# Kernel tuning notes

Hardware: AMD Instinct MI355X
Metric: run time of the kernel (lower is better)

The kernel has to match this reference:

```python
import jax, jax.numpy as jnp
import numpy as np

EPS = 1e-5

def _layer_norm(x, gamma, beta):
    mu = jnp.mean(x, axis=-1, keepdims=True)
    var = jnp.mean(jnp.square(x - mu), axis=-1, keepdims=True)
    return (x - mu) * jax.lax.rsqrt(var + EPS) * gamma + beta

def setup_inputs() -> dict:
    key = jax.random.key(0)
    ks = jax.random.split(key, 6)
    B, D, H = 8192, 1024, 1024
    x = jax.random.normal(ks[0], (B, D), dtype=jnp.float32)
    h0 = jax.random.normal(ks[1], (B, H), dtype=jnp.float32)
    c0 = jax.random.normal(ks[2], (B, H), dtype=jnp.float32)
    # learned params (orthogonal init approximated by scaled normal for reference purposes)
    weight_h = jax.random.normal(ks[3], (H, 4 * H), dtype=jnp.float32) / np.sqrt(H)
    weight_x = jax.random.normal(ks[4], (D, 4 * H), dtype=jnp.float32) / np.sqrt(D)
    bias = jnp.zeros((4 * H,), dtype=jnp.float32).at[:H].set(1.0)  # forget-gate bias init to 1
    ln1_g = jnp.ones((4 * H,), jnp.float32); ln1_b = jnp.zeros((4 * H,), jnp.float32)
    ln2_g = jnp.ones((4 * H,), jnp.float32); ln2_b = jnp.zeros((4 * H,), jnp.float32)
    ln3_g = jnp.ones((H,), jnp.float32); ln3_b = jnp.zeros((H,), jnp.float32)
    return {"x": x, "h0": h0, "c0": c0, "weight_h": weight_h, "weight_x": weight_x,
            "bias": bias, "ln1_g": ln1_g, "ln1_b": ln1_b, "ln2_g": ln2_g, "ln2_b": ln2_b,
            "ln3_g": ln3_g, "ln3_b": ln3_b}

def reference(x, h0, c0, weight_h, weight_x, bias, ln1_g, ln1_b, ln2_g, ln2_b, ln3_g, ln3_b):
    # gates: [B, 4H] = LN(h0 @ Wh) + LN(x @ Wx) + bias
    gates = _layer_norm(h0 @ weight_h, ln1_g, ln1_b) + _layer_norm(x @ weight_x, ln2_g, ln2_b) + bias
    H = h0.shape[-1]
    f_g, i_g, o_g, c_g = jnp.split(gates, 4, axis=1)  # forget, in, out, cell
    c1 = jax.nn.sigmoid(f_g) * c0 + jax.nn.sigmoid(i_g) * jnp.tanh(c_g)
    h1 = jax.nn.sigmoid(o_g) * jnp.tanh(_layer_norm(c1, ln3_g, ln3_b))
    return (h1, c1)
```

## Files before the change

### kernel.cpp

```cpp
#include <hip/hip_runtime.h>
#include <cstdint>

#define B_ROWS 8192
#define KDIM 1024
#define N4 4096

typedef __attribute__((ext_vector_type(8))) short short8;
typedef __attribute__((ext_vector_type(4))) float float4v;

__device__ __forceinline__ unsigned short f2bf(float f) {
  union { float f; unsigned int u; } v; v.f = f;
  unsigned int r = v.u + 0x7fffu + ((v.u >> 16) & 1u);
  return (unsigned short)(r >> 16);
}

__device__ __forceinline__ float bf2f(unsigned short s) {
  union { unsigned int u; float f; } v; v.u = ((unsigned int)s) << 16;
  return v.f;
}

__device__ __forceinline__ void async16(const unsigned short* g, unsigned short* l) {
  auto gp = (const __attribute__((address_space(1))) unsigned int*)(uintptr_t)g;
  auto lp = (__attribute__((address_space(3))) unsigned int*)(unsigned int)(uintptr_t)l;
  __builtin_amdgcn_global_load_lds(gp, lp, 16, 0, 0);
}

__device__ __forceinline__ float sigm(float v) {
  return __builtin_amdgcn_rcpf(1.f + __builtin_amdgcn_exp2f(-1.44269504088896f * v));
}
__device__ __forceinline__ float tanh_f(float v) {
  return 1.f - 2.f * __builtin_amdgcn_rcpf(1.f + __builtin_amdgcn_exp2f(2.88539008177793f * v));
}


__global__ __launch_bounds__(256) void cast_bf16(const float* __restrict__ in0,
                                                 unsigned short* __restrict__ out0,
                                                 const float* __restrict__ in1,
                                                 unsigned short* __restrict__ out1) {
  const float* in = blockIdx.y ? in1 : in0;
  unsigned short* out = blockIdx.y ? out1 : out0;
  int i = (blockIdx.x * 256 + threadIdx.x) * 4;
  float4 v = *(const float4*)(in + i);
  ushort4 o;
  o.x = f2bf(v.x); o.y = f2bf(v.y); o.z = f2bf(v.z); o.w = f2bf(v.w);
  *(ushort4*)(out + i) = o;
}

__global__ __launch_bounds__(256) void transpose_cast(const float* __restrict__ W0,
                                                      unsigned short* __restrict__ Wt0,
                                                      const float* __restrict__ W1,
                                                      unsigned short* __restrict__ Wt1) {
  const float* W = blockIdx.z ? W1 : W0;
  unsigned short* Wt = blockIdx.z ? Wt1 : Wt0;
  __shared__ float tile[32][33];
  int n0 = blockIdx.x * 32;
  int k0 = blockIdx.y * 32;
  int tx = threadIdx.x & 31;
  int ty = threadIdx.x >> 5;
#pragma unroll
  for (int i = 0; i < 32; i += 8)
    tile[ty + i][tx] = W[(size_t)(k0 + ty + i) * N4 + n0 + tx];
  __syncthreads();
#pragma unroll
  for (int i = 0; i < 32; i += 8)
    Wt[(size_t)(n0 + ty + i) * KDIM + k0 + tx] = f2bf(tile[tx][ty + i]);
}


#define BAR()    asm volatile("s_barrier" ::: "memory")
#define LGKM0()  asm volatile("s_waitcnt lgkmcnt(0)" ::: "memory")
#define VM4BAR() asm volatile("s_waitcnt vmcnt(4)\n\ts_barrier" ::: "memory")
#define SCHED0() __builtin_amdgcn_sched_barrier(0)

__global__ __launch_bounds__(512, 2) void gemm_bf16(
    const unsigned short* __restrict__ Ah, const unsigned short* __restrict__ Wth,
    unsigned short* __restrict__ Uh,
    const unsigned short* __restrict__ Ax, const unsigned short* __restrict__ Wtx,
    unsigned short* __restrict__ Ux, int row0) {
  const unsigned short* A; const unsigned short* W; unsigned short* U;
  if (blockIdx.z == 0) { A = Ah; W = Wth; U = Uh; } else { A = Ax; W = Wtx; U = Ux; }

  __shared__ unsigned short ldsA[2 * 256 * 64];
  __shared__ unsigned short ldsB[2 * 256 * 64];

  const int tid = threadIdx.x;
  const int wave = tid >> 6;
  const int lane = tid & 63;
  const int wm2 = wave >> 2;
  const int wn4 = wave & 3;

  const int gx = N4 / 256;
  const int nwg = gx * (int)gridDim.y;
  const int f = (int)blockIdx.y * gx + (int)blockIdx.x;
  const int qq = nwg >> 3, rr = nwg & 7;
  const int xcd = f & 7, idx = f >> 3;
  const int wg = (xcd < rr) ? (xcd * (qq + 1) + idx)
                            : (rr * (qq + 1) + (xcd - rr) * qq + idx);
  const int bx = wg & (gx - 1);
  const int by = wg / gx;

  const int m0 = row0 + by * 256;
  const int n0 = bx * 256;

  const int r8 = lane >> 3;
  const int c8 = lane & 7;
  const int g8 = ((c8 - r8) & 7) * 8;
  const int aE = (wave & 3) * 16 + (wave >> 2) * 128;
  const int aL = aE + 64;
  const int bE = (wave >> 1) * 64 + (wave & 1) * 16;
  const int bL = bE + 32;

  const unsigned short* gAe = A + (size_t)(m0 + aE + r8) * KDIM + g8;
  const unsigned short* gAl = A + (size_t)(m0 + aL + r8) * KDIM + g8;
  const unsigned short* gBe = W + (size_t)(n0 + bE + r8) * KDIM + g8;
  const unsigned short* gBl = W + (size_t)(n0 + bL + r8) * KDIM + g8;

  const int lq = lane & 15, lh = lane >> 4;
  const int offA0 = (wm2 * 128 + lq) * 64 + ((lh + lq) & 7) * 8;
  const int offA1 = (wm2 * 128 + lq) * 64 + ((4 + lh + lq) & 7) * 8;
  const int offB0 = (wn4 * 64 + lq) * 64 + ((lh + lq) & 7) * 8;
  const int offB1 = (wn4 * 64 + lq) * 64 + ((4 + lh + lq) & 7) * 8;

  float4v acc[8][4];
  float4v zero = {0.f, 0.f, 0.f, 0.f};
#pragma unroll
  for (int i = 0; i < 8; ++i)
#pragma unroll
    for (int j = 0; j < 4; ++j) acc[i][j] = zero;

#define STAGE2(gptr, lbase, kk)                                   \
  do {                                                            \
    async16((gptr) + (kk), (lbase));                              \
    async16((gptr) + (kk) + 8 * KDIM, (lbase) + 8 * 64);          \
  } while (0)

  STAGE2(gAe, ldsA + aE * 64, 0);
  STAGE2(gBe, ldsB + bE * 64, 0);
  STAGE2(gBl, ldsB + bL * 64, 0);
  STAGE2(gAl, ldsA + aL * 64, 0);
  VM4BAR();

  short8 aF[4][2], bF[4][2];

#pragma unroll 2
  for (int t = 0; t < KDIM / 64; ++t) {
    const unsigned short* sA = ldsA + (t & 1) * 16384;
    const unsigned short* sB = ldsB + (t & 1) * 16384;
    unsigned short* nA = (unsigned short*)ldsA + ((t + 1) & 1) * 16384;
    unsigned short* nB = (unsigned short*)ldsB + ((t + 1) & 1) * 16384;
    const int kNX = (t + 1) * 64;

#pragma unroll
    for (int mi = 0; mi < 4; ++mi) {
      aF[mi][0] = *(const short8*)(sA + offA0 + mi * 1024);
      aF[mi][1] = *(const short8*)(sA + offA1 + mi * 1024);
    }
#pragma unroll
    for (int ni = 0; ni < 2; ++ni) {
      bF[ni][0] = *(const short8*)(sB + offB0 + ni * 1024);
      bF[ni][1] = *(const short8*)(sB + offB1 + ni * 1024);
    }
    STAGE2(gAe, nA + aE * 64, kNX);
    BAR(); LGKM0(); SCHED0();
    __builtin_amdgcn_s_setprio(1);
#pragma unroll
    for (int kk = 0; kk < 2; ++kk)
#pragma unroll
      for (int mi = 0; mi < 4; ++mi)
#pragma unroll
        for (int ni = 0; ni < 2; ++ni)
          acc[mi][ni] = __builtin_amdgcn_mfma_f32_16x16x32_bf16(aF[mi][kk], bF[ni][kk], acc[mi][ni], 0, 0, 0);
    __builtin_amdgcn_s_setprio(0);
    SCHED0();
    VM4BAR();

#pragma unroll
    for (int ni = 0; ni < 2; ++ni) {
      bF[2 + ni][0] = *(const short8*)(sB + offB0 + (2 + ni) * 1024);
      bF[2 + ni][1] = *(const short8*)(sB + offB1 + (2 + ni) * 1024);
    }
    STAGE2(gBe, nB + bE * 64, kNX);
    BAR(); LGKM0(); SCHED0();
    __builtin_amdgcn_s_setprio(1);
#pragma unroll
    for (int kk = 0; kk < 2; ++kk)
#pragma unroll
      for (int mi = 0; mi < 4; ++mi)
#pragma unroll
        for (int ni = 0; ni < 2; ++ni)
          acc[mi][2 + ni] = __builtin_amdgcn_mfma_f32_16x16x32_bf16(aF[mi][kk], bF[2 + ni][kk], acc[mi][2 + ni], 0, 0, 0);
    __builtin_amdgcn_s_setprio(0);
    SCHED0();
    VM4BAR();

#pragma unroll
    for (int mi = 0; mi < 4; ++mi) {
      aF[mi][0] = *(const short8*)(sA + offA0 + (4 + mi) * 1024);
      aF[mi][1] = *(const short8*)(sA + offA1 + (4 + mi) * 1024);
    }
    STAGE2(gBl, nB + bL * 64, kNX);
    BAR(); LGKM0(); SCHED0();
    __builtin_amdgcn_s_setprio(1);
#pragma unroll
    for (int kk = 0; kk < 2; ++kk)
#pragma unroll
      for (int mi = 0; mi < 4; ++mi)
#pragma unroll
        for (int ni = 0; ni < 2; ++ni)
          acc[4 + mi][ni] = __builtin_amdgcn_mfma_f32_16x16x32_bf16(aF[mi][kk], bF[ni][kk], acc[4 + mi][ni], 0, 0, 0);
    __builtin_amdgcn_s_setprio(0);
    SCHED0();
    BAR();

    STAGE2(gAl, nA + aL * 64, kNX);
    BAR(); SCHED0();
    __builtin_amdgcn_s_setprio(1);
#pragma unroll
    for (int kk = 0; kk < 2; ++kk)
#pragma unroll
      for (int mi = 0; mi < 4; ++mi)
#pragma unroll
        for (int ni = 0; ni < 2; ++ni)
          acc[4 + mi][2 + ni] = __builtin_amdgcn_mfma_f32_16x16x32_bf16(aF[mi][kk], bF[2 + ni][kk], acc[4 + mi][2 + ni], 0, 0, 0);
    __builtin_amdgcn_s_setprio(0);
    SCHED0();
    VM4BAR();
  }
  asm volatile("s_waitcnt vmcnt(0)" ::: "memory");

  const int colc = lane & 15;
  const int rowq = (lane >> 4) * 4;
  unsigned short* Ub = U + (size_t)(by * 256 + wm2 * 128 + rowq) * N4 + n0 + wn4 * 64 + colc;
#pragma unroll
  for (int mi = 0; mi < 8; ++mi)
#pragma unroll
    for (int r = 0; r < 4; ++r) {
      unsigned short* Urow = Ub + (size_t)(mi * 16 + r) * N4;
#pragma unroll
      for (int ni = 0; ni < 4; ++ni) Urow[ni * 16] = f2bf(acc[mi][ni][r]);
    }
}


__global__ __launch_bounds__(256) void fused_ln_lstm(
    const unsigned short* __restrict__ Uh, const unsigned short* __restrict__ Ux,
    const float* __restrict__ c0, const float* __restrict__ bias,
    const float* __restrict__ g1, const float* __restrict__ b1,
    const float* __restrict__ g2, const float* __restrict__ b2,
    const float* __restrict__ g3, const float* __restrict__ b3,
    float* __restrict__ h1o, float* __restrict__ c1o, int row0) {
  const int t = threadIdx.x;
  const int lane = t & 63;
  const int wv = t >> 6;
  const size_t rloc = blockIdx.x;
  const size_t rabs = rloc + (size_t)row0;

  const ushort4* uh = (const ushort4*)(Uh + rloc * N4);
  const ushort4* ux = (const ushort4*)(Ux + rloc * N4);
  float4 cold = ((const float4*)(c0 + rabs * KDIM))[t];

  float4 vh[4], vx[4];
  float sh = 0.f, qh = 0.f, sx = 0.f, qx = 0.f;
#pragma unroll
  for (int k = 0; k < 4; ++k) {
    ushort4 au = uh[k * 256 + t];
    float4 a; a.x = bf2f(au.x); a.y = bf2f(au.y); a.z = bf2f(au.z); a.w = bf2f(au.w);
    vh[k] = a;
    sh += (a.x + a.y) + (a.z + a.w);
    qh += a.x * a.x + a.y * a.y + a.z * a.z + a.w * a.w;
    ushort4 bu = ux[k * 256 + t];
    float4 b; b.x = bf2f(bu.x); b.y = bf2f(bu.y); b.z = bf2f(bu.z); b.w = bf2f(bu.w);
    vx[k] = b;
    sx += (b.x + b.y) + (b.z + b.w);
    qx += b.x * b.x + b.y * b.y + b.z * b.z + b.w * b.w;
  }
  __shared__ float red[4][4];
#pragma unroll
  for (int o = 32; o > 0; o >>= 1) {
    sh += __shfl_down(sh, o); qh += __shfl_down(qh, o);
    sx += __shfl_down(sx, o); qx += __shfl_down(qx, o);
  }
  if (lane == 0) { red[wv][0] = sh; red[wv][1] = qh; red[wv][2] = sx; red[wv][3] = qx; }
  __syncthreads();
  sh = red[0][0] + red[1][0] + red[2][0] + red[3][0];
  qh = red[0][1] + red[1][1] + red[2][1] + red[3][1];
  sx = red[0][2] + red[1][2] + red[2][2] + red[3][2];
  qx = red[0][3] + red[1][3] + red[2][3] + red[3][3];
  const float inv4 = 1.f / 4096.f;
  const float muh = sh * inv4, mux = sx * inv4;
  const float rsh = rsqrtf(qh * inv4 - muh * muh + 1e-5f);
  const float rsx = rsqrtf(qx * inv4 - mux * mux + 1e-5f);

  float4 gate[4];
#pragma unroll
  for (int k = 0; k < 4; ++k) {
    int j = k * 256 + t;
    float4 G1 = ((const float4*)g1)[j], B1 = ((const float4*)b1)[j];
    float4 G2 = ((const float4*)g2)[j], B2 = ((const float4*)b2)[j];
    float4 BB = ((const float4*)bias)[j];
    float4 a = vh[k], b = vx[k], r;
    r.x = (a.x - muh) * rsh * G1.x + B1.x + (b.x - mux) * rsx * G2.x + B2.x + BB.x;
    r.y = (a.y - muh) * rsh * G1.y + B1.y + (b.y - mux) * rsx * G2.y + B2.y + BB.y;
    r.z = (a.z - muh) * rsh * G1.z + B1.z + (b.z - mux) * rsx * G2.z + B2.z + BB.z;
    r.w = (a.w - muh) * rsh * G1.w + B1.w + (b.w - mux) * rsx * G2.w + B2.w + BB.w;
    gate[k] = r;
  }
  float4 fg = gate[0], ig = gate[1], og = gate[2], cg = gate[3];
  float4 c1v;
  c1v.x = sigm(fg.x) * cold.x + sigm(ig.x) * tanh_f(cg.x);
  c1v.y = sigm(fg.y) * cold.y + sigm(ig.y) * tanh_f(cg.y);
  c1v.z = sigm(fg.z) * cold.z + sigm(ig.z) * tanh_f(cg.z);
  c1v.w = sigm(fg.w) * cold.w + sigm(ig.w) * tanh_f(cg.w);

  float sc = (c1v.x + c1v.y) + (c1v.z + c1v.w);
  float qc = c1v.x * c1v.x + c1v.y * c1v.y + c1v.z * c1v.z + c1v.w * c1v.w;
#pragma unroll
  for (int o = 32; o > 0; o >>= 1) { sc += __shfl_down(sc, o); qc += __shfl_down(qc, o); }
  __syncthreads();
  if (lane == 0) { red[wv][0] = sc; red[wv][1] = qc; }
  __syncthreads();
  sc = red[0][0] + red[1][0] + red[2][0] + red[3][0];
  qc = red[0][1] + red[1][1] + red[2][1] + red[3][1];
  const float invH = 1.f / 1024.f;
  const float muc = sc * invH;
  const float rsc = rsqrtf(qc * invH - muc * muc + 1e-5f);
  float4 G3 = ((const float4*)g3)[t], B3 = ((const float4*)b3)[t];
  float4 h1v;
  h1v.x = sigm(og.x) * tanh_f((c1v.x - muc) * rsc * G3.x + B3.x);
  h1v.y = sigm(og.y) * tanh_f((c1v.y - muc) * rsc * G3.y + B3.y);
  h1v.z = sigm(og.z) * tanh_f((c1v.z - muc) * rsc * G3.z + B3.z);
  h1v.w = sigm(og.w) * tanh_f((c1v.w - muc) * rsc * G3.w + B3.w);

  ((float4*)(h1o + rabs * KDIM))[t] = h1v;
  ((float4*)(c1o + rabs * KDIM))[t] = c1v;
}


extern "C" void kernel_launch(void* const* d_in, const int* in_sizes, int n_in,
                              void* d_out, int out_size, void* d_ws, size_t ws_size,
                              hipStream_t stream) {
  const float* x    = (const float*)d_in[0];
  const float* h0   = (const float*)d_in[1];
  const float* c0   = (const float*)d_in[2];
  const float* Wh   = (const float*)d_in[3];
  const float* Wx   = (const float*)d_in[4];
  const float* bias = (const float*)d_in[5];
  const float* g1   = (const float*)d_in[6];
  const float* b1   = (const float*)d_in[7];
  const float* g2   = (const float*)d_in[8];
  const float* b2   = (const float*)d_in[9];
  const float* g3   = (const float*)d_in[10];
  const float* b3   = (const float*)d_in[11];
  float* h1o = (float*)d_out;
  float* c1o = h1o + (size_t)B_ROWS * KDIM;

  unsigned short* Ah  = (unsigned short*)d_ws;
  unsigned short* Ax  = Ah + (size_t)B_ROWS * KDIM;
  unsigned short* Wth = Ax + (size_t)B_ROWS * KDIM;
  unsigned short* Wtx = Wth + (size_t)N4 * KDIM;
  unsigned short* U = Wtx + (size_t)N4 * KDIM;
  size_t used = ((size_t)B_ROWS * KDIM * 2 + (size_t)N4 * KDIM * 2) * sizeof(unsigned short);
  size_t rem = ws_size > used ? ws_size - used : 0;
  int chunk = (int)(rem / ((size_t)2 * N4 * sizeof(unsigned short)));
  chunk &= ~255;
  if (chunk > B_ROWS) chunk = B_ROWS;
  if (chunk < 256) chunk = 256;

  cast_bf16<<<dim3(B_ROWS * KDIM / 1024, 2), 256, 0, stream>>>(h0, Ah, x, Ax);
  transpose_cast<<<dim3(N4 / 32, KDIM / 32, 2), 256, 0, stream>>>(Wh, Wth, Wx, Wtx);

  for (int r0 = 0; r0 < B_ROWS; r0 += chunk) {
    int rows = chunk;
    if (r0 + rows > B_ROWS) rows = B_ROWS - r0;
    unsigned short* Uh = U;
    unsigned short* Ux = U + (size_t)rows * N4;
    gemm_bf16<<<dim3(N4 / 256, rows / 256, 2), 512, 0, stream>>>(Ah, Wth, Uh, Ax, Wtx, Ux, r0);
    fused_ln_lstm<<<rows, 256, 0, stream>>>(Uh, Ux, c0, bias, g1, b1, g2, b2, g3, b3, h1o, c1o, r0);
  }
}
```

Before: 366.7 us.

## Restructure GEMM main loop into two phases with deeper B prefetch

The GEMM inner loop goes from four sub-phases with partial fragment loads and barriers to two phases per K-tile. Each phase loads all A/B fragments for one k-half, and each wave stages 32 contiguous rows. B tiles are now prefetched two iterations ahead and A one ahead, which cuts barriers and waitcnts per iteration. Separately, the bf16 cast kernel and the weight transpose-cast kernel are merged into one launch. The cost is more fragment registers held per wave and a changed overlap pattern between loads and MFMAs.

```diff
diff --git a/kernel.cpp b/kernel.cpp
--- a/kernel.cpp
+++ b/kernel.cpp
@@ -33,44 +33,45 @@
 }
 
 
-__global__ __launch_bounds__(256) void cast_bf16(const float* __restrict__ in0,
-                                                 unsigned short* __restrict__ out0,
-                                                 const float* __restrict__ in1,
-                                                 unsigned short* __restrict__ out1) {
-  const float* in = blockIdx.y ? in1 : in0;
-  unsigned short* out = blockIdx.y ? out1 : out0;
-  int i = (blockIdx.x * 256 + threadIdx.x) * 4;
-  float4 v = *(const float4*)(in + i);
-  ushort4 o;
-  o.x = f2bf(v.x); o.y = f2bf(v.y); o.z = f2bf(v.z); o.w = f2bf(v.w);
-  *(ushort4*)(out + i) = o;
-}
-
-__global__ __launch_bounds__(256) void transpose_cast(const float* __restrict__ W0,
-                                                      unsigned short* __restrict__ Wt0,
-                                                      const float* __restrict__ W1,
-                                                      unsigned short* __restrict__ Wt1) {
-  const float* W = blockIdx.z ? W1 : W0;
-  unsigned short* Wt = blockIdx.z ? Wt1 : Wt0;
+__global__ __launch_bounds__(256) void prep(
+    const float* __restrict__ h0, const float* __restrict__ x,
+    unsigned short* __restrict__ Ah, unsigned short* __restrict__ Ax,
+    const float* __restrict__ Wh, const float* __restrict__ Wx,
+    unsigned short* __restrict__ Wth, unsigned short* __restrict__ Wtx) {
   __shared__ float tile[32][33];
-  int n0 = blockIdx.x * 32;
-  int k0 = blockIdx.y * 32;
-  int tx = threadIdx.x & 31;
-  int ty = threadIdx.x >> 5;
-#pragma unroll
-  for (int i = 0; i < 32; i += 8)
-    tile[ty + i][tx] = W[(size_t)(k0 + ty + i) * N4 + n0 + tx];
-  __syncthreads();
-#pragma unroll
-  for (int i = 0; i < 32; i += 8)
-    Wt[(size_t)(n0 + ty + i) * KDIM + k0 + tx] = f2bf(tile[tx][ty + i]);
-}
-
-
-#define BAR()    asm volatile("s_barrier" ::: "memory")
+  const int bid = blockIdx.x;
+  if (bid < 16384) {
+    const float* in = (bid >= 8192) ? x : h0;
+    unsigned short* out = (bid >= 8192) ? Ax : Ah;
+    int i = ((bid & 8191) * 256 + threadIdx.x) * 4;
+    float4 v = *(const float4*)(in + i);
+    ushort4 o;
+    o.x = f2bf(v.x); o.y = f2bf(v.y); o.z = f2bf(v.z); o.w = f2bf(v.w);
+    *(ushort4*)(out + i) = o;
+  } else {
+    int b2 = bid - 16384;
+    const float* W = (b2 >= 4096) ? Wx : Wh;
+    unsigned short* Wt = (b2 >= 4096) ? Wtx : Wth;
+    int r = b2 & 4095;
+    int n0 = (r & 127) * 32;
+    int k0 = (r >> 7) * 32;
+    int tx = threadIdx.x & 31;
+    int ty = threadIdx.x >> 5;
+#pragma unroll
+    for (int i = 0; i < 32; i += 8)
+      tile[ty + i][tx] = W[(size_t)(k0 + ty + i) * N4 + n0 + tx];
+    __syncthreads();
+#pragma unroll
+    for (int i = 0; i < 32; i += 8)
+      Wt[(size_t)(n0 + ty + i) * KDIM + k0 + tx] = f2bf(tile[tx][ty + i]);
+  }
+}
+
+
 #define LGKM0()  asm volatile("s_waitcnt lgkmcnt(0)" ::: "memory")
+#define SCHED0() __builtin_amdgcn_sched_barrier(0)
+#define BARRIER() __builtin_amdgcn_s_barrier()
 #define VM4BAR() asm volatile("s_waitcnt vmcnt(4)\n\ts_barrier" ::: "memory")
-#define SCHED0() __builtin_amdgcn_sched_barrier(0)
 
 __global__ __launch_bounds__(512, 2) void gemm_bf16(
     const unsigned short* __restrict__ Ah, const unsigned short* __restrict__ Wth,
@@ -105,15 +106,11 @@
   const int r8 = lane >> 3;
   const int c8 = lane & 7;
   const int g8 = ((c8 - r8) & 7) * 8;
-  const int aE = (wave & 3) * 16 + (wave >> 2) * 128;
-  const int aL = aE + 64;
-  const int bE = (wave >> 1) * 64 + (wave & 1) * 16;
-  const int bL = bE + 32;
-
-  const unsigned short* gAe = A + (size_t)(m0 + aE + r8) * KDIM + g8;
-  const unsigned short* gAl = A + (size_t)(m0 + aL + r8) * KDIM + g8;
-  const unsigned short* gBe = W + (size_t)(n0 + bE + r8) * KDIM + g8;
-  const unsigned short* gBl = W + (size_t)(n0 + bL + r8) * KDIM + g8;
+  const int aR = wave * 32;
+  const int bR = wave * 32;
+
+  const unsigned short* gA = A + (size_t)(m0 + aR + r8) * KDIM + g8;
+  const unsigned short* gB = W + (size_t)(n0 + bR + r8) * KDIM + g8;
 
   const int lq = lane & 15, lh = lane >> 4;
   const int offA0 = (wm2 * 128 + lq) * 64 + ((lh + lq) & 7) * 8;
@@ -128,102 +125,61 @@
 #pragma unroll
     for (int j = 0; j < 4; ++j) acc[i][j] = zero;
 
-#define STAGE2(gptr, lbase, kk)                                   \
+#define STAGE4(gp, lb, kk)                                        \
   do {                                                            \
-    async16((gptr) + (kk), (lbase));                              \
-    async16((gptr) + (kk) + 8 * KDIM, (lbase) + 8 * 64);          \
+    async16((gp) + (kk), (lb));                                   \
+    async16((gp) + (kk) + 8 * KDIM, (lb) + 8 * 64);               \
+    async16((gp) + (kk) + 16 * KDIM, (lb) + 16 * 64);             \
+    async16((gp) + (kk) + 24 * KDIM, (lb) + 24 * 64);             \
   } while (0)
 
-  STAGE2(gAe, ldsA + aE * 64, 0);
-  STAGE2(gBe, ldsB + bE * 64, 0);
-  STAGE2(gBl, ldsB + bL * 64, 0);
-  STAGE2(gAl, ldsA + aL * 64, 0);
+  STAGE4(gB, ldsB + bR * 64, 0);
+  STAGE4(gA, ldsA + aR * 64, 0);
+  STAGE4(gB, ldsB + 16384 + bR * 64, 64);
   VM4BAR();
 
-  short8 aF[4][2], bF[4][2];
-
-#pragma unroll 2
+  short8 aF0[8], aF1[8], bF0[4], bF1[4];
+
   for (int t = 0; t < KDIM / 64; ++t) {
     const unsigned short* sA = ldsA + (t & 1) * 16384;
     const unsigned short* sB = ldsB + (t & 1) * 16384;
     unsigned short* nA = (unsigned short*)ldsA + ((t + 1) & 1) * 16384;
-    unsigned short* nB = (unsigned short*)ldsB + ((t + 1) & 1) * 16384;
-    const int kNX = (t + 1) * 64;
-
-#pragma unroll
-    for (int mi = 0; mi < 4; ++mi) {
-      aF[mi][0] = *(const short8*)(sA + offA0 + mi * 1024);
-      aF[mi][1] = *(const short8*)(sA + offA1 + mi * 1024);
-    }
-#pragma unroll
-    for (int ni = 0; ni < 2; ++ni) {
-      bF[ni][0] = *(const short8*)(sB + offB0 + ni * 1024);
-      bF[ni][1] = *(const short8*)(sB + offB1 + ni * 1024);
-    }
-    STAGE2(gAe, nA + aE * 64, kNX);
-    BAR(); LGKM0(); SCHED0();
+    unsigned short* cB = (unsigned short*)ldsB + (t & 1) * 16384;
+    const int kA = (t + 1) * 64;
+    const int kB = (t + 2) * 64;
+
+    STAGE4(gA, nA + aR * 64, kA);
+
+#pragma unroll
+    for (int mi = 0; mi < 8; ++mi) aF0[mi] = *(const short8*)(sA + offA0 + mi * 1024);
+#pragma unroll
+    for (int nj = 0; nj < 4; ++nj) bF0[nj] = *(const short8*)(sB + offB0 + nj * 1024);
+#pragma unroll
+    for (int mi = 0; mi < 8; ++mi) aF1[mi] = *(const short8*)(sA + offA1 + mi * 1024);
+#pragma unroll
+    for (int nj = 0; nj < 4; ++nj) bF1[nj] = *(const short8*)(sB + offB1 + nj * 1024);
+
     __builtin_amdgcn_s_setprio(1);
 #pragma unroll
-    for (int kk = 0; kk < 2; ++kk)
-#pragma unroll
-      for (int mi = 0; mi < 4; ++mi)
-#pragma unroll
-        for (int ni = 0; ni < 2; ++ni)
-          acc[mi][ni] = __builtin_amdgcn_mfma_f32_16x16x32_bf16(aF[mi][kk], bF[ni][kk], acc[mi][ni], 0, 0, 0);
+    for (int mi = 0; mi < 8; ++mi)
+#pragma unroll
+      for (int nj = 0; nj < 4; ++nj)
+        acc[mi][nj] = __builtin_amdgcn_mfma_f32_16x16x32_bf16(aF0[mi], bF0[nj], acc[mi][nj], 0, 0, 0);
     __builtin_amdgcn_s_setprio(0);
-    SCHED0();
-    VM4BAR();
-
-#pragma unroll
-    for (int ni = 0; ni < 2; ++ni) {
-      bF[2 + ni][0] = *(const short8*)(sB + offB0 + (2 + ni) * 1024);
-      bF[2 + ni][1] = *(const short8*)(sB + offB1 + (2 + ni) * 1024);
-    }
-    STAGE2(gBe, nB + bE * 64, kNX);
-    BAR(); LGKM0(); SCHED0();
+
+    LGKM0(); SCHED0();
+    BARRIER();
+
+    STAGE4(gB, cB + bR * 64, kB);
+
     __builtin_amdgcn_s_setprio(1);
 #pragma unroll
-    for (int kk = 0; kk < 2; ++kk)
-#pragma unroll
-      for (int mi = 0; mi < 4; ++mi)
-#pragma unroll
-        for (int ni = 0; ni < 2; ++ni)
-          acc[mi][2 + ni] = __builtin_amdgcn_mfma_f32_16x16x32_bf16(aF[mi][kk], bF[2 + ni][kk], acc[mi][2 + ni], 0, 0, 0);
+    for (int mi = 0; mi < 8; ++mi)
+#pragma unroll
+      for (int nj = 0; nj < 4; ++nj)
+        acc[mi][nj] = __builtin_amdgcn_mfma_f32_16x16x32_bf16(aF1[mi], bF1[nj], acc[mi][nj], 0, 0, 0);
     __builtin_amdgcn_s_setprio(0);
-    SCHED0();
-    VM4BAR();
-
-#pragma unroll
-    for (int mi = 0; mi < 4; ++mi) {
-      aF[mi][0] = *(const short8*)(sA + offA0 + (4 + mi) * 1024);
-      aF[mi][1] = *(const short8*)(sA + offA1 + (4 + mi) * 1024);
-    }
-    STAGE2(gBl, nB + bL * 64, kNX);
-    BAR(); LGKM0(); SCHED0();
-    __builtin_amdgcn_s_setprio(1);
-#pragma unroll
-    for (int kk = 0; kk < 2; ++kk)
-#pragma unroll
-      for (int mi = 0; mi < 4; ++mi)
-#pragma unroll
-        for (int ni = 0; ni < 2; ++ni)
-          acc[4 + mi][ni] = __builtin_amdgcn_mfma_f32_16x16x32_bf16(aF[mi][kk], bF[ni][kk], acc[4 + mi][ni], 0, 0, 0);
-    __builtin_amdgcn_s_setprio(0);
-    SCHED0();
-    BAR();
-
-    STAGE2(gAl, nA + aL * 64, kNX);
-    BAR(); SCHED0();
-    __builtin_amdgcn_s_setprio(1);
-#pragma unroll
-    for (int kk = 0; kk < 2; ++kk)
-#pragma unroll
-      for (int mi = 0; mi < 4; ++mi)
-#pragma unroll
-        for (int ni = 0; ni < 2; ++ni)
-          acc[4 + mi][2 + ni] = __builtin_amdgcn_mfma_f32_16x16x32_bf16(aF[mi][kk], bF[2 + ni][kk], acc[4 + mi][2 + ni], 0, 0, 0);
-    __builtin_amdgcn_s_setprio(0);
-    SCHED0();
+
     VM4BAR();
   }
   asm volatile("s_waitcnt vmcnt(0)" ::: "memory");
@@ -237,7 +193,7 @@
     for (int r = 0; r < 4; ++r) {
       unsigned short* Urow = Ub + (size_t)(mi * 16 + r) * N4;
 #pragma unroll
-      for (int ni = 0; ni < 4; ++ni) Urow[ni * 16] = f2bf(acc[mi][ni][r]);
+      for (int nj = 0; nj < 4; ++nj) Urow[nj * 16] = f2bf(acc[mi][nj][r]);
     }
 }
 
@@ -366,8 +322,7 @@
   if (chunk > B_ROWS) chunk = B_ROWS;
   if (chunk < 256) chunk = 256;
 
-  cast_bf16<<<dim3(B_ROWS * KDIM / 1024, 2), 256, 0, stream>>>(h0, Ah, x, Ax);
-  transpose_cast<<<dim3(N4 / 32, KDIM / 32, 2), 256, 0, stream>>>(Wh, Wth, Wx, Wtx);
+  prep<<<24576, 256, 0, stream>>>(h0, x, Ah, Ax, Wh, Wx, Wth, Wtx);
 
   for (int r0 = 0; r0 < B_ROWS; r0 += chunk) {
     int rows = chunk;
```

New measurement: 368.8 us. No clear change (+0.6%).
